# Kernel tuning notes

Hardware: AMD Instinct MI355X
Metric: run time of the kernel (lower is better)

## Reference

```python
import jax, jax.numpy as jnp
import numpy as np

N = 100000          # num nodes
E = 1600000         # num edges
IN_F = 256
OUT_F = 256
D_LABEL = 32
ALPHA = 0.2         # LeakyReLU negative slope
EPS = 1e-9


def setup_inputs() -> dict:
    key = jax.random.key(0)
    k1, k2, k3, k4 = jax.random.split(key, 4)
    h = jax.random.normal(k1, (N, IN_F), dtype=jnp.float32)
    label = jax.random.normal(k2, (N, D_LABEL), dtype=jnp.float32)
    # xavier_uniform with gain=1.414 on [IN_F, OUT_F]
    limit = 1.414 * np.sqrt(6.0 / (IN_F + OUT_F))
    W = jax.random.uniform(k3, (IN_F, OUT_F), dtype=jnp.float32,
                           minval=-limit, maxval=limit)
    adj_indices = jax.random.randint(k4, (2, E), 0, N, dtype=jnp.int64)
    return {"h": h, "label": label, "W": W, "adj_indices": adj_indices}


def reference(h, label, W, adj_indices):
    src = adj_indices[0]  # [E]
    dst = adj_indices[1]  # [E]
    Wh = h @ W  # [N, OUT_F]
    # edge attention logits: leakyrelu(<label[src], label[dst]>)
    e = jnp.sum(label[src] * label[dst], axis=1)            # [E]
    e = jnp.where(e >= 0, e, ALPHA * e)                     # LeakyReLU
    # segment softmax over rows (src)
    exp_e = jnp.exp(e)                                      # [E]
    row_sum = jax.ops.segment_sum(exp_e, src, num_segments=N)  # [N]
    row_sum = jnp.maximum(row_sum, EPS)
    att = exp_e / row_sum[src]                              # [E]
    # dropout is identity at inference (training=False)
    # sparse-dense matmul: h_prime[i] = sum_{(i,j) in edges} att * Wh[j]
    msgs = att[:, None] * Wh[dst]                           # [E, OUT_F]
    h_prime = jax.ops.segment_sum(msgs, src, num_segments=N)  # [N, OUT_F]
    return h_prime  # concat=False -> no ELU
```

## Files before the change

### kernel.cpp

```cpp
#include <hip/hip_runtime.h>
#include <hip/hip_bf16.h>

#define NNODES 100000
#define NEDGES 1600000
#define ALPHA  0.2f
#define EPSV   1e-9f

typedef __bf16 bf16x8 __attribute__((ext_vector_type(8)));
typedef float  f32x4  __attribute__((ext_vector_type(4)));
typedef unsigned short u16x8 __attribute__((ext_vector_type(8)));

static __device__ inline unsigned short f2bf(float f) {
    unsigned int u = __float_as_uint(f);
    unsigned int r = u + 0x7fff + ((u >> 16) & 1);
    return (unsigned short)(r >> 16);
}
static __device__ inline float bf2f(unsigned short v) {
    return __uint_as_float((unsigned int)v << 16);
}

__global__ void k_zero(int* __restrict__ p, int n) {
    int i = blockIdx.x * blockDim.x + threadIdx.x;
    if (i < n) p[i] = 0;
}

__global__ void k_prepw(const float* __restrict__ W, unsigned short* __restrict__ Wt) {
    const int i = blockIdx.x * 256 + threadIdx.x;
    const int n = i >> 8, k = i & 255;
    Wt[i] = f2bf(W[k * 256 + n]);
}

#define BM 128
#define BK 32
#define LSTRIDE 40
__global__ __launch_bounds__(256, 2) void k_gemm(const float* __restrict__ h,
                                                 const unsigned short* __restrict__ Wt,
                                                 unsigned short* __restrict__ Wh) {
    __shared__ __align__(16) unsigned short As[BM * LSTRIDE];
    __shared__ __align__(16) unsigned short Bs[256 * LSTRIDE];
    const int tid  = threadIdx.x;
    const int m0   = blockIdx.x * BM;
    const int wave = tid >> 6;
    const int lane = tid & 63;
    const int wm = (wave & 1) * 64;
    const int wn = (wave >> 1) * 128;
    const int fm = lane & 15;
    const int fq = lane >> 4;
    const int fk = fq * 8;

    f32x4 acc[4][8];
    const f32x4 z = {0.f, 0.f, 0.f, 0.f};
#pragma unroll
    for (int i = 0; i < 4; ++i)
#pragma unroll
        for (int j = 0; j < 8; ++j) acc[i][j] = z;

    const int arow = tid >> 1;
    const int acol = (tid & 1) * 16;
    const bool arow_ok = (m0 + arow) < NNODES;
    const float* hrow = h + (size_t)(m0 + arow) * 256 + acol;

    for (int kc = 0; kc < 256; kc += BK) {
        float4 a0, a1, a2, a3;
        if (arow_ok) {
            a0 = *(const float4*)(hrow + kc + 0);
            a1 = *(const float4*)(hrow + kc + 4);
            a2 = *(const float4*)(hrow + kc + 8);
            a3 = *(const float4*)(hrow + kc + 12);
        } else {
            a0 = a1 = a2 = a3 = make_float4(0.f, 0.f, 0.f, 0.f);
        }
        u16x8 bv[4];
#pragma unroll
        for (int q = 0; q < 4; ++q) {
            const int c = tid + 256 * q;
            const int n = c >> 2, koff = (c & 3) * 8;
            bv[q] = *(const u16x8*)(Wt + n * 256 + kc + koff);
        }
        __syncthreads();
        u16x8 p0, p1;
        p0[0]=f2bf(a0.x); p0[1]=f2bf(a0.y); p0[2]=f2bf(a0.z); p0[3]=f2bf(a0.w);
        p0[4]=f2bf(a1.x); p0[5]=f2bf(a1.y); p0[6]=f2bf(a1.z); p0[7]=f2bf(a1.w);
        p1[0]=f2bf(a2.x); p1[1]=f2bf(a2.y); p1[2]=f2bf(a2.z); p1[3]=f2bf(a2.w);
        p1[4]=f2bf(a3.x); p1[5]=f2bf(a3.y); p1[6]=f2bf(a3.z); p1[7]=f2bf(a3.w);
        *(u16x8*)&As[arow * LSTRIDE + acol]     = p0;
        *(u16x8*)&As[arow * LSTRIDE + acol + 8] = p1;
#pragma unroll
        for (int q = 0; q < 4; ++q) {
            const int c = tid + 256 * q;
            const int n = c >> 2, koff = (c & 3) * 8;
            *(u16x8*)&Bs[n * LSTRIDE + koff] = bv[q];
        }
        __syncthreads();
        bf16x8 af[4], bfr[8];
#pragma unroll
        for (int i = 0; i < 4; ++i)
            af[i] = __builtin_bit_cast(bf16x8,
                *(const u16x8*)&As[(wm + 16 * i + fm) * LSTRIDE + fk]);
#pragma unroll
        for (int j = 0; j < 8; ++j)
            bfr[j] = __builtin_bit_cast(bf16x8,
                *(const u16x8*)&Bs[(wn + 16 * j + fm) * LSTRIDE + fk]);
#pragma unroll
        for (int i = 0; i < 4; ++i)
#pragma unroll
            for (int j = 0; j < 8; ++j)
                acc[i][j] = __builtin_amdgcn_mfma_f32_16x16x32_bf16(af[i], bfr[j], acc[i][j], 0, 0, 0);
    }
#pragma unroll
    for (int i = 0; i < 4; ++i) {
#pragma unroll
        for (int r = 0; r < 4; ++r) {
            const int grow = m0 + wm + 16 * i + fq * 4 + r;
            if (grow < NNODES) {
                unsigned short* orow = Wh + (size_t)grow * 256 + wn + fm;
#pragma unroll
                for (int j = 0; j < 8; ++j)
                    orow[16 * j] = f2bf(acc[i][j][r]);
            }
        }
    }
}

__global__ __launch_bounds__(256) void k_attn(const float* __restrict__ label,
                       const int* __restrict__ src,
                       const int* __restrict__ dst,
                       float* __restrict__ exp_e,
                       int* __restrict__ pos_in_row,
                       int* __restrict__ counts) {
    const int t = blockIdx.x * 256 + threadIdx.x;
    const int e = t >> 2;
    const int l4 = t & 3;
    if (e >= NEDGES) return;
    const int s = src[e], d = dst[e];
    const float4* ls = (const float4*)&label[s * 32 + l4 * 8];
    const float4* ld = (const float4*)&label[d * 32 + l4 * 8];
    const float4 a0 = ls[0], a1 = ls[1];
    const float4 b0 = ld[0], b1 = ld[1];
    float dot = a0.x * b0.x + a0.y * b0.y + a0.z * b0.z + a0.w * b0.w
              + a1.x * b1.x + a1.y * b1.y + a1.z * b1.z + a1.w * b1.w;
    dot += __shfl_xor(dot, 1);
    dot += __shfl_xor(dot, 2);
    if (l4 == 0) {
        const float lr = dot >= 0.f ? dot : ALPHA * dot;
        exp_e[e] = expf(lr);
        pos_in_row[e] = atomicAdd(&counts[s], 1);
    }
}

__global__ __launch_bounds__(256) void k_scan1(const int* __restrict__ counts,
                                               int* __restrict__ row_start,
                                               int* __restrict__ blockSums) {
    __shared__ int ssum[256];
    const int tid = threadIdx.x;
    const int base = blockIdx.x * 1024 + tid * 4;
    int v[4];
#pragma unroll
    for (int c = 0; c < 4; ++c) v[c] = (base + c < NNODES) ? counts[base + c] : 0;
    const int s = v[0] + v[1] + v[2] + v[3];
    ssum[tid] = s;
    __syncthreads();
    for (int off = 1; off < 256; off <<= 1) {
        const int t = (tid >= off) ? ssum[tid - off] : 0;
        __syncthreads();
        ssum[tid] += t;
        __syncthreads();
    }
    if (tid == 255) blockSums[blockIdx.x] = ssum[255];
    int p = ssum[tid] - s;
#pragma unroll
    for (int c = 0; c < 4; ++c) {
        if (base + c < NNODES) row_start[base + c] = p;
        p += v[c];
    }
}

__global__ __launch_bounds__(256) void k_scan2(int* __restrict__ blockSums, int nb) {
    __shared__ int ssum[256];
    const int tid = threadIdx.x;
    const int s = (tid < nb) ? blockSums[tid] : 0;
    ssum[tid] = s;
    __syncthreads();
    for (int off = 1; off < 256; off <<= 1) {
        const int t = (tid >= off) ? ssum[tid - off] : 0;
        __syncthreads();
        ssum[tid] += t;
        __syncthreads();
    }
    if (tid < nb) blockSums[tid] = ssum[tid] - s;
}

__global__ void k_scan3(int* __restrict__ row_start, const int* __restrict__ blockSums) {
    const int i = blockIdx.x * blockDim.x + threadIdx.x;
    if (i < NNODES) row_start[i] += blockSums[i >> 10];
}

__global__ void k_scatter(const int* __restrict__ src,
                          const int* __restrict__ dst,
                          const float* __restrict__ exp_e,
                          const int* __restrict__ pos_in_row,
                          const int* __restrict__ row_start,
                          uint2* __restrict__ sorted_pack) {
    const int e = blockIdx.x * blockDim.x + threadIdx.x;
    if (e >= NEDGES) return;
    const int pos = row_start[src[e]] + pos_in_row[e];
    sorted_pack[pos] = make_uint2((unsigned)dst[e], __float_as_uint(exp_e[e]));
}

__global__ __launch_bounds__(256) void k_aggregate(const unsigned short* __restrict__ Wh,
                                                   const int* __restrict__ row_start,
                                                   const uint2* __restrict__ sorted_pack,
                                                   float* __restrict__ out) {
    const int node = blockIdx.x * 8 + (threadIdx.x >> 5);
    if (node >= NNODES) return;
    const int sub = threadIdx.x & 31;
    const int rs = row_start[node];
    const int re = (node == NNODES - 1) ? NEDGES : row_start[node + 1];
    const unsigned short* __restrict__ Whc = Wh + sub * 8;
    float acc[8] = {0.f, 0.f, 0.f, 0.f, 0.f, 0.f, 0.f, 0.f};
    float wsum = 0.f;
    int i = rs;
    for (; i + 4 <= re; i += 4) {
        const uint2 p0 = sorted_pack[i + 0];
        const uint2 p1 = sorted_pack[i + 1];
        const uint2 p2 = sorted_pack[i + 2];
        const uint2 p3 = sorted_pack[i + 3];
        const u16x8 v0 = *(const u16x8*)&Whc[(size_t)p0.x * 256];
        const u16x8 v1 = *(const u16x8*)&Whc[(size_t)p1.x * 256];
        const u16x8 v2 = *(const u16x8*)&Whc[(size_t)p2.x * 256];
        const u16x8 v3 = *(const u16x8*)&Whc[(size_t)p3.x * 256];
        const float w0 = __uint_as_float(p0.y), w1 = __uint_as_float(p1.y);
        const float w2 = __uint_as_float(p2.y), w3 = __uint_as_float(p3.y);
        wsum += (w0 + w1) + (w2 + w3);
#pragma unroll
        for (int c = 0; c < 8; ++c) {
            acc[c] = fmaf(w0, bf2f(v0[c]), acc[c]);
            acc[c] = fmaf(w1, bf2f(v1[c]), acc[c]);
            acc[c] = fmaf(w2, bf2f(v2[c]), acc[c]);
            acc[c] = fmaf(w3, bf2f(v3[c]), acc[c]);
        }
    }
    for (; i < re; ++i) {
        const uint2 p = sorted_pack[i];
        const u16x8 v = *(const u16x8*)&Whc[(size_t)p.x * 256];
        const float w = __uint_as_float(p.y);
        wsum += w;
#pragma unroll
        for (int c = 0; c < 8; ++c) acc[c] = fmaf(w, bf2f(v[c]), acc[c]);
    }
    const float inv = 1.f / fmaxf(wsum, EPSV);
    float4 o0 = make_float4(acc[0] * inv, acc[1] * inv, acc[2] * inv, acc[3] * inv);
    float4 o1 = make_float4(acc[4] * inv, acc[5] * inv, acc[6] * inv, acc[7] * inv);
    float* orow = out + (size_t)node * 256 + sub * 8;
    *(float4*)(orow + 0) = o0;
    *(float4*)(orow + 4) = o1;
}

extern "C" void kernel_launch(void* const* d_in, const int* in_sizes, int n_in,
                              void* d_out, int out_size, void* d_ws, size_t ws_size,
                              hipStream_t stream) {
    const float* h     = (const float*)d_in[0];
    const float* label = (const float*)d_in[1];
    const float* W     = (const float*)d_in[2];
    const int*   adj   = (const int*)d_in[3];
    const int* src = adj;
    const int* dst = adj + NEDGES;
    float* out = (float*)d_out;

    char* ws = (char*)d_ws;
    unsigned short* Wh  = (unsigned short*)(ws + 0);
    unsigned short* Wt  = (unsigned short*)(ws + 51200000);
    float* exp_e        = (float*)(ws + 51400000);
    int*   pos_in_row   = (int*)  (ws + 57800000);
    uint2* sorted_pack  = (uint2*)(ws + 64200000);
    int*   counts       = (int*)  (ws + 77000000);
    int*   row_start    = (int*)  (ws + 77400000);
    int*   blockSums    = (int*)  (ws + 77800000);

    k_zero<<<(NNODES + 255) / 256, 256, 0, stream>>>(counts, NNODES);
    k_prepw<<<256, 256, 0, stream>>>(W, Wt);
    k_gemm<<<(NNODES + BM - 1) / BM, 256, 0, stream>>>(h, Wt, Wh);
    k_attn<<<(4 * NEDGES + 255) / 256, 256, 0, stream>>>(label, src, dst, exp_e, pos_in_row, counts);

    const int nb = (NNODES + 1023) / 1024;
    k_scan1<<<nb, 256, 0, stream>>>(counts, row_start, blockSums);
    k_scan2<<<1, 256, 0, stream>>>(blockSums, nb);
    k_scan3<<<(NNODES + 255) / 256, 256, 0, stream>>>(row_start, blockSums);

    k_scatter<<<(NEDGES + 255) / 256, 256, 0, stream>>>(src, dst, exp_e, pos_in_row,
                                                        row_start, sorted_pack);
    k_aggregate<<<(NNODES + 7) / 8, 256, 0, stream>>>(Wh, row_start, sorted_pack, out);
}
```

Before: 428.9 us.

## Count edges first, fuse attention with CSR scatter, merge zero/prep kernels

Restructures the CSR build. A lightweight count pass runs first and the scan follows, so the attention kernel can compute exp logits and write directly into the sorted position by atomically decrementing the per-row counts. This removes the exp_e and pos_in_row intermediate arrays and the separate scatter pass. The zero and weight-prep kernels are merged, and the aggregate loop gains an 8-wide unrolled batch of gathers for more memory-level parallelism. The cost is an extra read of src and extra atomics, plus more register pressure in the aggregation kernel.

```diff
diff --git a/kernel.cpp b/kernel.cpp
--- a/kernel.cpp
+++ b/kernel.cpp
@@ -19,15 +19,20 @@
     return __uint_as_float((unsigned int)v << 16);
 }
 
-__global__ void k_zero(int* __restrict__ p, int n) {
-    int i = blockIdx.x * blockDim.x + threadIdx.x;
-    if (i < n) p[i] = 0;
-}
-
-__global__ void k_prepw(const float* __restrict__ W, unsigned short* __restrict__ Wt) {
+__global__ void k_zero_prep(int* __restrict__ counts,
+                            const float* __restrict__ W,
+                            unsigned short* __restrict__ Wt) {
     const int i = blockIdx.x * 256 + threadIdx.x;
-    const int n = i >> 8, k = i & 255;
-    Wt[i] = f2bf(W[k * 256 + n]);
+    if (i < NNODES) counts[i] = 0;
+    if (i < 65536) {
+        const int n = i >> 8, k = i & 255;
+        Wt[i] = f2bf(W[k * 256 + n]);
+    }
+}
+
+__global__ void k_count(const int* __restrict__ src, int* __restrict__ counts) {
+    const int e = blockIdx.x * 256 + threadIdx.x;
+    if (e < NEDGES) atomicAdd(&counts[src[e]], 1);
 }
 
 #define BM 128
@@ -122,12 +127,59 @@
     }
 }
 
-__global__ __launch_bounds__(256) void k_attn(const float* __restrict__ label,
-                       const int* __restrict__ src,
-                       const int* __restrict__ dst,
-                       float* __restrict__ exp_e,
-                       int* __restrict__ pos_in_row,
-                       int* __restrict__ counts) {
+__global__ __launch_bounds__(256) void k_scan1(const int* __restrict__ counts,
+                                               int* __restrict__ row_start,
+                                               int* __restrict__ blockSums) {
+    __shared__ int ssum[256];
+    const int tid = threadIdx.x;
+    const int base = blockIdx.x * 1024 + tid * 4;
+    int v[4];
+#pragma unroll
+    for (int c = 0; c < 4; ++c) v[c] = (base + c < NNODES) ? counts[base + c] : 0;
+    const int s = v[0] + v[1] + v[2] + v[3];
+    ssum[tid] = s;
+    __syncthreads();
+    for (int off = 1; off < 256; off <<= 1) {
+        const int t = (tid >= off) ? ssum[tid - off] : 0;
+        __syncthreads();
+        ssum[tid] += t;
+        __syncthreads();
+    }
+    if (tid == 255) blockSums[blockIdx.x] = ssum[255];
+    int p = ssum[tid] - s;
+#pragma unroll
+    for (int c = 0; c < 4; ++c) {
+        if (base + c < NNODES) row_start[base + c] = p;
+        p += v[c];
+    }
+}
+
+__global__ __launch_bounds__(256) void k_scan2(int* __restrict__ blockSums, int nb) {
+    __shared__ int ssum[256];
+    const int tid = threadIdx.x;
+    const int s = (tid < nb) ? blockSums[tid] : 0;
+    ssum[tid] = s;
+    __syncthreads();
+    for (int off = 1; off < 256; off <<= 1) {
+        const int t = (tid >= off) ? ssum[tid - off] : 0;
+        __syncthreads();
+        ssum[tid] += t;
+        __syncthreads();
+    }
+    if (tid < nb) blockSums[tid] = ssum[tid] - s;
+}
+
+__global__ void k_scan3(int* __restrict__ row_start, const int* __restrict__ blockSums) {
+    const int i = blockIdx.x * blockDim.x + threadIdx.x;
+    if (i < NNODES) row_start[i] += blockSums[i >> 10];
+}
+
+__global__ __launch_bounds__(256) void k_attn_scatter(const float* __restrict__ label,
+                                                      const int* __restrict__ src,
+                                                      const int* __restrict__ dst,
+                                                      const int* __restrict__ row_start,
+                                                      int* __restrict__ counts,
+                                                      uint2* __restrict__ sorted_pack) {
     const int t = blockIdx.x * 256 + threadIdx.x;
     const int e = t >> 2;
     const int l4 = t & 3;
@@ -143,68 +195,10 @@
     dot += __shfl_xor(dot, 2);
     if (l4 == 0) {
         const float lr = dot >= 0.f ? dot : ALPHA * dot;
-        exp_e[e] = expf(lr);
-        pos_in_row[e] = atomicAdd(&counts[s], 1);
-    }
-}
-
-__global__ __launch_bounds__(256) void k_scan1(const int* __restrict__ counts,
-                                               int* __restrict__ row_start,
-                                               int* __restrict__ blockSums) {
-    __shared__ int ssum[256];
-    const int tid = threadIdx.x;
-    const int base = blockIdx.x * 1024 + tid * 4;
-    int v[4];
-#pragma unroll
-    for (int c = 0; c < 4; ++c) v[c] = (base + c < NNODES) ? counts[base + c] : 0;
-    const int s = v[0] + v[1] + v[2] + v[3];
-    ssum[tid] = s;
-    __syncthreads();
-    for (int off = 1; off < 256; off <<= 1) {
-        const int t = (tid >= off) ? ssum[tid - off] : 0;
-        __syncthreads();
-        ssum[tid] += t;
-        __syncthreads();
-    }
-    if (tid == 255) blockSums[blockIdx.x] = ssum[255];
-    int p = ssum[tid] - s;
-#pragma unroll
-    for (int c = 0; c < 4; ++c) {
-        if (base + c < NNODES) row_start[base + c] = p;
-        p += v[c];
-    }
-}
-
-__global__ __launch_bounds__(256) void k_scan2(int* __restrict__ blockSums, int nb) {
-    __shared__ int ssum[256];
-    const int tid = threadIdx.x;
-    const int s = (tid < nb) ? blockSums[tid] : 0;
-    ssum[tid] = s;
-    __syncthreads();
-    for (int off = 1; off < 256; off <<= 1) {
-        const int t = (tid >= off) ? ssum[tid - off] : 0;
-        __syncthreads();
-        ssum[tid] += t;
-        __syncthreads();
-    }
-    if (tid < nb) blockSums[tid] = ssum[tid] - s;
-}
-
-__global__ void k_scan3(int* __restrict__ row_start, const int* __restrict__ blockSums) {
-    const int i = blockIdx.x * blockDim.x + threadIdx.x;
-    if (i < NNODES) row_start[i] += blockSums[i >> 10];
-}
-
-__global__ void k_scatter(const int* __restrict__ src,
-                          const int* __restrict__ dst,
-                          const float* __restrict__ exp_e,
-                          const int* __restrict__ pos_in_row,
-                          const int* __restrict__ row_start,
-                          uint2* __restrict__ sorted_pack) {
-    const int e = blockIdx.x * blockDim.x + threadIdx.x;
-    if (e >= NEDGES) return;
-    const int pos = row_start[src[e]] + pos_in_row[e];
-    sorted_pack[pos] = make_uint2((unsigned)dst[e], __float_as_uint(exp_e[e]));
+        const float ex = expf(lr);
+        const int pos = row_start[s] + atomicSub(&counts[s], 1) - 1;
+        sorted_pack[pos] = make_uint2((unsigned)d, __float_as_uint(ex));
+    }
 }
 
 __global__ __launch_bounds__(256) void k_aggregate(const unsigned short* __restrict__ Wh,
@@ -220,24 +214,34 @@
     float acc[8] = {0.f, 0.f, 0.f, 0.f, 0.f, 0.f, 0.f, 0.f};
     float wsum = 0.f;
     int i = rs;
+    for (; i + 8 <= re; i += 8) {
+        uint2 p[8];
+        u16x8 v[8];
+#pragma unroll
+        for (int u = 0; u < 8; ++u) p[u] = sorted_pack[i + u];
+#pragma unroll
+        for (int u = 0; u < 8; ++u) v[u] = *(const u16x8*)&Whc[(size_t)p[u].x * 256];
+#pragma unroll
+        for (int u = 0; u < 8; ++u) {
+            const float w = __uint_as_float(p[u].y);
+            wsum += w;
+#pragma unroll
+            for (int c = 0; c < 8; ++c) acc[c] = fmaf(w, bf2f(v[u][c]), acc[c]);
+        }
+    }
     for (; i + 4 <= re; i += 4) {
-        const uint2 p0 = sorted_pack[i + 0];
-        const uint2 p1 = sorted_pack[i + 1];
-        const uint2 p2 = sorted_pack[i + 2];
-        const uint2 p3 = sorted_pack[i + 3];
-        const u16x8 v0 = *(const u16x8*)&Whc[(size_t)p0.x * 256];
-        const u16x8 v1 = *(const u16x8*)&Whc[(size_t)p1.x * 256];
-        const u16x8 v2 = *(const u16x8*)&Whc[(size_t)p2.x * 256];
-        const u16x8 v3 = *(const u16x8*)&Whc[(size_t)p3.x * 256];
-        const float w0 = __uint_as_float(p0.y), w1 = __uint_as_float(p1.y);
-        const float w2 = __uint_as_float(p2.y), w3 = __uint_as_float(p3.y);
-        wsum += (w0 + w1) + (w2 + w3);
-#pragma unroll
-        for (int c = 0; c < 8; ++c) {
-            acc[c] = fmaf(w0, bf2f(v0[c]), acc[c]);
-            acc[c] = fmaf(w1, bf2f(v1[c]), acc[c]);
-            acc[c] = fmaf(w2, bf2f(v2[c]), acc[c]);
-            acc[c] = fmaf(w3, bf2f(v3[c]), acc[c]);
+        uint2 p[4];
+        u16x8 v[4];
+#pragma unroll
+        for (int u = 0; u < 4; ++u) p[u] = sorted_pack[i + u];
+#pragma unroll
+        for (int u = 0; u < 4; ++u) v[u] = *(const u16x8*)&Whc[(size_t)p[u].x * 256];
+#pragma unroll
+        for (int u = 0; u < 4; ++u) {
+            const float w = __uint_as_float(p[u].y);
+            wsum += w;
+#pragma unroll
+            for (int c = 0; c < 8; ++c) acc[c] = fmaf(w, bf2f(v[u][c]), acc[c]);
         }
     }
     for (; i < re; ++i) {
@@ -270,24 +274,22 @@
     char* ws = (char*)d_ws;
     unsigned short* Wh  = (unsigned short*)(ws + 0);
     unsigned short* Wt  = (unsigned short*)(ws + 51200000);
-    float* exp_e        = (float*)(ws + 51400000);
-    int*   pos_in_row   = (int*)  (ws + 57800000);
-    uint2* sorted_pack  = (uint2*)(ws + 64200000);
-    int*   counts       = (int*)  (ws + 77000000);
-    int*   row_start    = (int*)  (ws + 77400000);
-    int*   blockSums    = (int*)  (ws + 77800000);
-
-    k_zero<<<(NNODES + 255) / 256, 256, 0, stream>>>(counts, NNODES);
-    k_prepw<<<256, 256, 0, stream>>>(W, Wt);
-    k_gemm<<<(NNODES + BM - 1) / BM, 256, 0, stream>>>(h, Wt, Wh);
-    k_attn<<<(4 * NEDGES + 255) / 256, 256, 0, stream>>>(label, src, dst, exp_e, pos_in_row, counts);
+    uint2* sorted_pack  = (uint2*)(ws + 51400064);
+    int*   counts       = (int*)  (ws + 64200064);
+    int*   row_start    = (int*)  (ws + 64600064);
+    int*   blockSums    = (int*)  (ws + 65000064);
+
+    k_zero_prep<<<(NNODES + 255) / 256, 256, 0, stream>>>(counts, W, Wt);
+    k_count<<<(NEDGES + 255) / 256, 256, 0, stream>>>(src, counts);
 
     const int nb = (NNODES + 1023) / 1024;
     k_scan1<<<nb, 256, 0, stream>>>(counts, row_start, blockSums);
     k_scan2<<<1, 256, 0, stream>>>(blockSums, nb);
     k_scan3<<<(NNODES + 255) / 256, 256, 0, stream>>>(row_start, blockSums);
 
-    k_scatter<<<(NEDGES + 255) / 256, 256, 0, stream>>>(src, dst, exp_e, pos_in_row,
-                                                        row_start, sorted_pack);
+    k_gemm<<<(NNODES + BM - 1) / BM, 256, 0, stream>>>(h, Wt, Wh);
+
+    k_attn_scatter<<<(4 * NEDGES + 255) / 256, 256, 0, stream>>>(label, src, dst,
+                                                                 row_start, counts, sorted_pack);
     k_aggregate<<<(NNODES + 7) / 8, 256, 0, stream>>>(Wh, row_start, sorted_pack, out);
 }
```

Measured after the change: 493.4 us. 15.0% more time.
